# Kernel optimization log

Hardware: AMD Instinct MI355X
Metric: run time of the kernel (lower is better)

## Reference

```python
import jax, jax.numpy as jnp
import numpy as np


def setup_inputs() -> dict:
    key = jax.random.key(0)
    ks = jax.random.split(key, 16)
    N, F_in, C, E = 50000, 128, 64, 800000
    H = 2 * C      # hidden width of first GCN layer = 128
    P = 128        # num_proj_hidden
    K = 3          # cluster_num (hardcoded in GRACE)

    def lin(kw, fan_in, fan_out):
        # torch Linear default init: U(-1/sqrt(fan_in), 1/sqrt(fan_in))
        bound = 1.0 / np.sqrt(fan_in)
        return jax.random.uniform(kw, (fan_in, fan_out), jnp.float32, -bound, bound)

    inp = {
        "x1": jax.random.normal(ks[0], (N, F_in), jnp.float32),
        "edge_index1": jax.random.randint(ks[1], (2, E), 0, N, jnp.int64 if jax.config.jax_enable_x64 else jnp.int32),
        "x2": jax.random.normal(ks[2], (N, F_in), jnp.float32),
        "edge_index2": jax.random.randint(ks[3], (2, E), 0, N, jnp.int64 if jax.config.jax_enable_x64 else jnp.int32),
        # encoder GCN layers
        "W1": lin(ks[4], F_in, H), "b1": jnp.zeros((H,), jnp.float32),
        "W2": lin(ks[5], H, C),    "b2": jnp.zeros((C,), jnp.float32),
        # instance projector: Linear(C,C) -> ReLU -> Linear(C,P)
        "Wp1": lin(ks[6], C, C), "bp1": jnp.zeros((C,), jnp.float32),
        "Wp2": lin(ks[7], C, P), "bp2": jnp.zeros((P,), jnp.float32),
        # cluster projector: Linear(C,C) -> ReLU -> Linear(C,K) -> Softmax
        "Wc1": lin(ks[8], C, C), "bc1": jnp.zeros((C,), jnp.float32),
        "Wc2": lin(ks[9], C, K), "bc2": jnp.zeros((K,), jnp.float32),
    }
    return inp


def _gcn_encoder(x, edge_index, W1, b1, W2, b2):
    N = x.shape[0]
    loop = jnp.arange(N, dtype=edge_index.dtype)
    row = jnp.concatenate([edge_index[0], loop])  # message sources (x_j)
    col = jnp.concatenate([edge_index[1], loop])  # aggregation targets
    deg = jax.ops.segment_sum(jnp.ones_like(col, jnp.float32), col, num_segments=N)
    dinv = jax.lax.rsqrt(deg)  # deg >= 1 due to self loops
    norm = dinv[row] * dinv[col]  # [E+N]

    def layer(h, W, b):
        h = h @ W  # transform first (PyG GCNConv), [N, F_out]
        msg = h[row] * norm[:, None]  # gather + scale, [E+N, F_out]
        return jax.ops.segment_sum(msg, col, num_segments=N) + b

    h = jax.nn.relu(layer(x, W1, b1))
    h = jax.nn.relu(layer(h, W2, b2))
    return h


def _l2norm(z, eps=1e-12):
    # matches F.normalize(z, dim=1): x / max(||x||, eps)
    n = jnp.sqrt(jnp.sum(z * z, axis=1, keepdims=True))
    return z / jnp.maximum(n, eps)


def reference(x1, edge_index1, x2, edge_index2,
              W1, b1, W2, b2, Wp1, bp1, Wp2, bp2, Wc1, bc1, Wc2, bc2):
    z1 = _gcn_encoder(x1, edge_index1, W1, b1, W2, b2)
    z2 = _gcn_encoder(x2, edge_index2, W1, b1, W2, b2)

    inst = lambda z: _l2norm(jax.nn.relu(z @ Wp1 + bp1) @ Wp2 + bp2)
    clus = lambda z: jax.nn.softmax(jax.nn.relu(z @ Wc1 + bc1) @ Wc2 + bc2, axis=1)

    z_i = inst(z1)
    z_j = inst(z2)
    c_i = clus(z1)
    c_j = clus(z2)
    return (z_i, z_j, c_i, c_j)
```

## Files before the change

### kernel.cpp

```cpp
#include <hip/hip_runtime.h>
#include <cstdint>
#include <cstddef>

using u16 = unsigned short;
using u32 = unsigned int;

typedef __bf16 bf16x8 __attribute__((ext_vector_type(8)));
typedef float  f32x4  __attribute__((ext_vector_type(4)));

__device__ __forceinline__ float bf2f(u16 b) { union { u32 i; float f; } v; v.i = ((u32)b) << 16; return v.f; }
__device__ __forceinline__ u16 f2bf(float f) { __bf16 b = (__bf16)f; return __builtin_bit_cast(u16, b); }
__device__ __forceinline__ float bflo(u32 u) { union { u32 i; float f; } v; v.i = u << 16; return v.f; }
__device__ __forceinline__ float bfhi(u32 u) { union { u32 i; float f; } v; v.i = u & 0xffff0000u; return v.f; }
__device__ __forceinline__ u32 pack2(float a, float b) { return (u32)f2bf(a) | ((u32)f2bf(b) << 16); }

__device__ __forceinline__ float loadx(const void* p, size_t i, int flag_bf16) {
    return flag_bf16 ? bf2f(((const u16*)p)[i]) : ((const float*)p)[i];
}
__device__ __forceinline__ void storex(void* p, size_t i, float v, int flag_bf16) {
    if (flag_bf16) ((u16*)p)[i] = f2bf(v);
    else           ((float*)p)[i] = v;
}

__device__ __forceinline__ bf16x8 load_afrag_ext(const void* A, size_t off, int flag) {
    if (flag) return *reinterpret_cast<const bf16x8*>((const u16*)A + off);
    const float* f = (const float*)A + off;
    float4 a = *reinterpret_cast<const float4*>(f);
    float4 b = *reinterpret_cast<const float4*>(f + 4);
    bf16x8 r;
    r[0] = (__bf16)a.x; r[1] = (__bf16)a.y; r[2] = (__bf16)a.z; r[3] = (__bf16)a.w;
    r[4] = (__bf16)b.x; r[5] = (__bf16)b.y; r[6] = (__bf16)b.z; r[7] = (__bf16)b.w;
    return r;
}

__global__ void k_detect(const u32* __restrict__ x, int* __restrict__ flag) {
    int lane = threadIdx.x;
    u32 u = x[lane];
    int e = (u >> 7) & 0xFF;
    int hit = (e >= 100 && e <= 145) ? 1 : 0;
    unsigned long long b = __ballot(hit);
    if (lane == 0) flag[0] = (__popcll(b) >= 32) ? 1 : 0;
}

struct ConvJob { const void* src; float* dst; int n; };
struct ConvJobs { ConvJob j[12]; };

__global__ void k_wconv(ConvJobs jobs, const int* __restrict__ flagp) {
    const int f = *flagp;
    const int stride = gridDim.x * blockDim.x;
    for (int s = 0; s < 12; ++s) {
        const ConvJob jb = jobs.j[s];
        for (int i = blockIdx.x * blockDim.x + threadIdx.x; i < jb.n; i += stride)
            jb.dst[i] = loadx(jb.src, i, f);
    }
}

struct TJob { const float* W; u16* WT; int K, NC; };
struct TJobs { TJob j[5]; };

__global__ void k_wtrans(TJobs jobs) {
    const int stride = gridDim.x * blockDim.x;
    for (int s = 0; s < 5; ++s) {
        const TJob jb = jobs.j[s];
        const int tot = jb.K * jb.NC;
        for (int i = blockIdx.x * blockDim.x + threadIdx.x; i < tot; i += stride) {
            int k = i / jb.NC, n = i - k * jb.NC;
            jb.WT[n * jb.K + k] = f2bf(jb.W[i]);
        }
    }
}

static const int CAPSH = 12;
static const int OVCAP = 65536;

__global__ __launch_bounds__(256) void k_bin(const int* __restrict__ ei0, const int* __restrict__ ei1,
                                             int* __restrict__ cur, u32* __restrict__ stage,
                                             int2* __restrict__ ov, int* __restrict__ ocnt,
                                             int E, int NB, int nblk) {
    const int g = blockIdx.y;
    const int* ei = g ? ei1 : ei0;
    const int chunk = (E + nblk - 1) / nblk;
    const int e0 = blockIdx.x * chunk;
    const int e1 = (e0 + chunk < E) ? e0 + chunk : E;
    const int tid = threadIdx.x;
    __shared__ int h[512];
    __shared__ int lb[512];
    for (int i = tid; i < NB; i += 256) h[i] = 0;
    __syncthreads();
    for (int e = e0 + tid; e < e1; e += 256) {
        int d = __builtin_nontemporal_load(ei + E + e);
        atomicAdd(&h[d >> 7], 1);
    }
    __syncthreads();
    for (int b = tid; b < NB; b += 256) {
        int c = h[b];
        lb[b] = c ? atomicAdd(&cur[g * NB + b], c) : 0;
    }
    __syncthreads();
    for (int i = tid; i < NB; i += 256) h[i] = 0;
    __syncthreads();
    for (int e = e0 + tid; e < e1; e += 256) {
        int s = __builtin_nontemporal_load(ei + e);
        int d = ei[E + e];
        int b = d >> 7;
        int p = lb[b] + atomicAdd(&h[b], 1);
        if (p < (1 << CAPSH)) {
            stage[((size_t)(g * NB + b) << CAPSH) + p] = (u32)s | ((u32)(d & 127) << 16);
        } else {
            int oi = atomicAdd(ocnt, 1);
            if (oi < OVCAP) ov[oi] = make_int2(s, d | (g << 24));
        }
    }
}

__global__ __launch_bounds__(256) void k_bscan(const int* __restrict__ cur, const int2* __restrict__ ov,
                                               const int* __restrict__ ocnt, int* __restrict__ bbase,
                                               int* __restrict__ rowptr, int N, int E, int NB) {
    __shared__ int tot[2][512];
    const int tid = threadIdx.x;
    for (int g = 0; g < 2; ++g)
        for (int i = tid; i < 512; i += 256) {
            int s = 0;
            if (i < NB) {
                int cv = cur[g * NB + i];
                s = (cv < (1 << CAPSH)) ? cv : (1 << CAPSH);
            }
            tot[g][i] = s;
        }
    __syncthreads();
    int no = *ocnt; if (no > OVCAP) no = OVCAP;
    for (int i = tid; i < no; i += 256) {
        int y = ov[i].y;
        atomicAdd(&tot[y >> 24][(y & 0xFFFFFF) >> 7], 1);
    }
    __syncthreads();
    int o00 = tot[0][tid], o01 = tot[0][tid + 256];
    int o10 = tot[1][tid], o11 = tot[1][tid + 256];
    for (int off = 1; off < 512; off <<= 1) {
        int a0 = tot[0][tid]       + ((tid >= off)       ? tot[0][tid - off]       : 0);
        int a1 = tot[0][tid + 256] + ((tid + 256 >= off) ? tot[0][tid + 256 - off] : 0);
        int b0 = tot[1][tid]       + ((tid >= off)       ? tot[1][tid - off]       : 0);
        int b1 = tot[1][tid + 256] + ((tid + 256 >= off) ? tot[1][tid + 256 - off] : 0);
        __syncthreads();
        tot[0][tid] = a0; tot[0][tid + 256] = a1;
        tot[1][tid] = b0; tot[1][tid + 256] = b1;
        __syncthreads();
    }
    if (tid < NB)       { bbase[tid]            = tot[0][tid] - o00;       bbase[NB + tid]       = tot[1][tid] - o10; }
    if (tid + 256 < NB) { bbase[tid + 256]      = tot[0][tid + 256] - o01; bbase[NB + tid + 256] = tot[1][tid + 256] - o11; }
    if (tid == 0) {
        rowptr[N] = E;
        rowptr[(size_t)(N + 1) + N] = E;
    }
}

__global__ __launch_bounds__(256) void k_scatter(const int* __restrict__ cur, const u32* __restrict__ stage,
                                                 const int2* __restrict__ ov, const int* __restrict__ ocnt,
                                                 const int* __restrict__ bbase, int* __restrict__ rowptr,
                                                 float* __restrict__ dinv, int* __restrict__ csr,
                                                 int N, int E, int NB) {
    const int g = blockIdx.y, b = blockIdx.x, tid = threadIdx.x;
    const int lo = b << 7;
    int R = N - lo; if (R > 128) R = 128;
    __shared__ int hist[128], scn[128], curs[128];
    if (tid < 128) hist[tid] = 0;
    __syncthreads();
    int cv = cur[g * NB + b];
    const int n = (cv < (1 << CAPSH)) ? cv : (1 << CAPSH);
    const u32* sp = stage + ((size_t)(g * NB + b) << CAPSH);
    for (int i = tid; i < n; i += 256) atomicAdd(&hist[sp[i] >> 16], 1);
    int no = *ocnt; if (no > OVCAP) no = OVCAP;
    for (int i = tid; i < no; i += 256) {
        int y = ov[i].y;
        if ((y >> 24) != g) continue;
        int d = y & 0xFFFFFF;
        if (d >= lo && d < lo + 128) atomicAdd(&hist[d - lo], 1);
    }
    __syncthreads();
    int orig = (tid < 128) ? hist[tid] : 0;
    if (tid < 128) scn[tid] = orig;
    __syncthreads();
    for (int off = 1; off < 128; off <<= 1) {
        int v = 0;
        if (tid < 128) v = scn[tid] + ((tid >= off) ? scn[tid - off] : 0);
        __syncthreads();
        if (tid < 128) scn[tid] = v;
        __syncthreads();
    }
    const int base = bbase[g * NB + b];
    if (tid < R) {
        int ex = base + scn[tid] - orig;
        rowptr[(size_t)g * (N + 1) + lo + tid] = ex;
        curs[tid] = ex;
        dinv[(size_t)g * N + lo + tid] = rsqrtf((float)(orig + 1));
    }
    __syncthreads();
    int* out = csr + (size_t)g * E;
    for (int i = tid; i < n; i += 256) {
        u32 v = sp[i];
        int pos = atomicAdd(&curs[v >> 16], 1);
        out[pos] = (int)(v & 0xFFFFu);
    }
    for (int i = tid; i < no; i += 256) {
        int y = ov[i].y;
        if ((y >> 24) != g) continue;
        int d = y & 0xFFFFFF;
        if (d >= lo && d < lo + 128) {
            int pos = atomicAdd(&curs[d - lo], 1);
            out[pos] = ov[i].x;
        }
    }
}

template <int K, int NC, bool AEXT, bool BIAS, bool RELU, bool NORM, bool OEXT>
__global__ __launch_bounds__(256) void k_mgemm(const void* __restrict__ A0, const void* __restrict__ A1,
                                               size_t astride, const u16* __restrict__ WT,
                                               const float* __restrict__ bias, void* __restrict__ outv,
                                               size_t out_off, size_t ostride, int M,
                                               const int* __restrict__ flagp) {
    constexpr int NT = NC / 16;
    constexpr int KI = K / 32;
    const int flag = *flagp;
    const int g = blockIdx.y;
    const void* Av = g ? A1 : A0;
    const int lane = threadIdx.x & 63;
    const int wave = threadIdx.x >> 6;
    const int q = lane >> 4;
    const int c = lane & 15;
    const int m0 = blockIdx.x * 64 + wave * 16;
    int arow = m0 + c;
    if (arow > M - 1) arow = M - 1;
    const size_t abase = (size_t)g * astride + (size_t)arow * K;

    bf16x8 afr[KI];
#pragma unroll
    for (int ki = 0; ki < KI; ++ki) {
        size_t off = abase + (size_t)ki * 32 + q * 8;
        if (AEXT) afr[ki] = load_afrag_ext(Av, off, flag);
        else      afr[ki] = *reinterpret_cast<const bf16x8*>((const u16*)Av + off);
    }

    f32x4 acc[NT];
#pragma unroll
    for (int t = 0; t < NT; ++t) acc[t] = (f32x4){0.f, 0.f, 0.f, 0.f};

#pragma unroll
    for (int ki = 0; ki < KI; ++ki) {
#pragma unroll
        for (int t = 0; t < NT; ++t) {
            const u16* bptr = WT + (size_t)(t * 16 + c) * K + ki * 32 + q * 8;
            bf16x8 bfr = *reinterpret_cast<const bf16x8*>(bptr);
            acc[t] = __builtin_amdgcn_mfma_f32_16x16x32_bf16(afr[ki], bfr, acc[t], 0, 0, 0);
        }
    }

#pragma unroll
    for (int t = 0; t < NT; ++t) {
        float bv = BIAS ? bias[t * 16 + c] : 0.f;
#pragma unroll
        for (int r = 0; r < 4; ++r) {
            float v = acc[t][r] + bv;
            if (RELU) v = fmaxf(v, 0.f);
            acc[t][r] = v;
        }
    }

    if constexpr (NORM) {
        float ss[4] = {0.f, 0.f, 0.f, 0.f};
#pragma unroll
        for (int t = 0; t < NT; ++t)
#pragma unroll
            for (int r = 0; r < 4; ++r) ss[r] += acc[t][r] * acc[t][r];
#pragma unroll
        for (int r = 0; r < 4; ++r) {
#pragma unroll
            for (int m = 1; m < 16; m <<= 1) ss[r] += __shfl_xor(ss[r], m, 64);
            float s = 1.f / fmaxf(sqrtf(ss[r]), 1e-12f);
#pragma unroll
            for (int t = 0; t < NT; ++t) acc[t][r] *= s;
        }
    }

    const size_t obase = out_off + (size_t)g * ostride;
#pragma unroll
    for (int r = 0; r < 4; ++r) {
        const int grow = m0 + q * 4 + r;
        if (grow < M) {
#pragma unroll
            for (int t = 0; t < NT; ++t) {
                size_t oi = obase + (size_t)grow * NC + t * 16 + c;
                if (OEXT) storex(outv, oi, acc[t][r], flag);
                else      ((u16*)outv)[oi] = f2bf(acc[t][r]);
            }
        }
    }
}

__global__ __launch_bounds__(256) void k_agg128(const u32* __restrict__ H, const int* __restrict__ rowptr,
                                                const int* __restrict__ csr, const float* __restrict__ dinv,
                                                const float* __restrict__ bias, u32* __restrict__ out,
                                                int N, int E) {
    const int g = blockIdx.y;
    const int node = blockIdx.x * 4 + (threadIdx.x >> 6);
    if (node >= N) return;
    const int lane = threadIdx.x & 63;
    const u32* h = H + (size_t)g * N * 64;
    const int* rp = rowptr + (size_t)g * (N + 1);
    const int* cs = csr + (size_t)g * E;
    const float* dv = dinv + (size_t)g * N;
    const float dn = dv[node];
    int e = rp[node];
    const int end = rp[node + 1];
    u32 su = h[(size_t)node * 64 + lane];
    float w = dn * dn;
    float a0 = bflo(su) * w, a1 = bfhi(su) * w;
    while (e + 8 <= end) {
        int sx[8];
#pragma unroll
        for (int j = 0; j < 8; ++j) sx[j] = cs[e + j];
        u32 hv[8]; float ws[8];
#pragma unroll
        for (int j = 0; j < 8; ++j) { hv[j] = h[(size_t)sx[j] * 64 + lane]; ws[j] = dv[sx[j]]; }
#pragma unroll
        for (int j = 0; j < 8; ++j) {
            float wj = ws[j] * dn;
            a0 += bflo(hv[j]) * wj;
            a1 += bfhi(hv[j]) * wj;
        }
        e += 8;
    }
    while (e + 2 <= end) {
        int s0 = cs[e], s1 = cs[e + 1];
        u32 h0 = h[(size_t)s0 * 64 + lane];
        u32 h1 = h[(size_t)s1 * 64 + lane];
        float w0 = dv[s0] * dn, w1 = dv[s1] * dn;
        a0 += bflo(h0) * w0; a1 += bfhi(h0) * w0;
        a0 += bflo(h1) * w1; a1 += bfhi(h1) * w1;
        e += 2;
    }
    if (e < end) {
        int s0 = cs[e];
        float w0 = dv[s0] * dn;
        u32 h0 = h[(size_t)s0 * 64 + lane];
        a0 += bflo(h0) * w0; a1 += bfhi(h0) * w0;
    }
    a0 = fmaxf(a0 + bias[2 * lane], 0.f);
    a1 = fmaxf(a1 + bias[2 * lane + 1], 0.f);
    out[((size_t)g * N + node) * 64 + lane] = pack2(a0, a1);
}

__global__ __launch_bounds__(256) void k_agg64(const u16* __restrict__ H, const int* __restrict__ rowptr,
                                               const int* __restrict__ csr, const float* __restrict__ dinv,
                                               const float* __restrict__ bias, u16* __restrict__ out,
                                               int N, int E) {
    const int g = blockIdx.y;
    const int node = blockIdx.x * 4 + (threadIdx.x >> 6);
    if (node >= N) return;
    const int lane = threadIdx.x & 63;
    const u16* h = H + (size_t)g * N * 64;
    const int* rp = rowptr + (size_t)g * (N + 1);
    const int* cs = csr + (size_t)g * E;
    const float* dv = dinv + (size_t)g * N;
    const float dn = dv[node];
    int e = rp[node];
    const int end = rp[node + 1];
    float a0 = bf2f(h[(size_t)node * 64 + lane]) * dn * dn;
    while (e + 8 <= end) {
        int sx[8];
#pragma unroll
        for (int j = 0; j < 8; ++j) sx[j] = cs[e + j];
        u16 hv[8]; float ws[8];
#pragma unroll
        for (int j = 0; j < 8; ++j) { hv[j] = h[(size_t)sx[j] * 64 + lane]; ws[j] = dv[sx[j]]; }
#pragma unroll
        for (int j = 0; j < 8; ++j) a0 += bf2f(hv[j]) * (ws[j] * dn);
        e += 8;
    }
    while (e + 2 <= end) {
        int s0 = cs[e], s1 = cs[e + 1];
        float h0 = bf2f(h[(size_t)s0 * 64 + lane]);
        float h1 = bf2f(h[(size_t)s1 * 64 + lane]);
        a0 += h0 * (dv[s0] * dn) + h1 * (dv[s1] * dn);
        e += 2;
    }
    if (e < end) {
        int s0 = cs[e];
        a0 += bf2f(h[(size_t)s0 * 64 + lane]) * (dv[s0] * dn);
    }
    a0 = fmaxf(a0 + bias[lane], 0.f);
    out[((size_t)g * N + node) * 64 + lane] = f2bf(a0);
}

__global__ __launch_bounds__(256) void k_clus(const u16* __restrict__ v, const float* __restrict__ Wc2,
                                              const float* __restrict__ bc2, void* __restrict__ outv,
                                              size_t out_off, size_t ostride, int N,
                                              const int* __restrict__ flagp) {
    const int g = blockIdx.y;
    const int node = blockIdx.x * 4 + (threadIdx.x >> 6);
    if (node >= N) return;
    const int flag = *flagp;
    const int lane = threadIdx.x & 63;
    float ul = bf2f(v[((size_t)g * N + node) * 64 + lane]);
    float a0 = ul * Wc2[lane * 3 + 0];
    float a1 = ul * Wc2[lane * 3 + 1];
    float a2 = ul * Wc2[lane * 3 + 2];
#pragma unroll
    for (int m = 1; m < 64; m <<= 1) {
        a0 += __shfl_xor(a0, m, 64);
        a1 += __shfl_xor(a1, m, 64);
        a2 += __shfl_xor(a2, m, 64);
    }
    a0 += bc2[0]; a1 += bc2[1]; a2 += bc2[2];
    float mx = fmaxf(a0, fmaxf(a1, a2));
    float e0 = expf(a0 - mx), e1 = expf(a1 - mx), e2 = expf(a2 - mx);
    float inv = 1.f / (e0 + e1 + e2);
    if (lane < 3) {
        float r = (lane == 0) ? e0 : ((lane == 1) ? e1 : e2);
        storex(outv, out_off + (size_t)g * ostride + (size_t)node * 3 + lane, r * inv, flag);
    }
}

extern "C" void kernel_launch(void* const* d_in, const int* in_sizes, int n_in,
                              void* d_out, int out_size, void* d_ws, size_t ws_size,
                              hipStream_t stream) {
    const int N = in_sizes[0] / 128;
    const int E = in_sizes[1] / 2;
    const int* ei0 = (const int*)d_in[1];
    const int* ei1 = (const int*)d_in[3];
    const int NB = (N + 127) >> 7;

    size_t off = 0;
    auto alloc = [&](size_t bytes) -> void* {
        void* p = (char*)d_ws + off;
        off += (bytes + 255) & ~(size_t)255;
        return p;
    };
    int* flag = (int*)alloc(256);
    const int wcnt[12] = {128 * 128, 128, 128 * 64, 64, 64 * 64, 64, 64 * 128, 128, 64 * 64, 64, 64 * 3, 3};
    float* wf[12];
    for (int i = 0; i < 12; ++i) wf[i] = (float*)alloc((size_t)wcnt[i] * 4);
    float* b1f = wf[1]; float* b2f = wf[3]; float* bp1f = wf[5]; float* bp2f = wf[7];
    float* bc1f = wf[9]; float* Wc2f = wf[10]; float* bc2f = wf[11];
    u16* W1T  = (u16*)alloc(128 * 128 * 2);
    u16* W2T  = (u16*)alloc(64 * 128 * 2);
    u16* Wp1T = (u16*)alloc(64 * 64 * 2);
    u16* Wp2T = (u16*)alloc(128 * 64 * 2);
    u16* Wc1T = (u16*)alloc(64 * 64 * 2);

    const int ncell = 2 * NB;
    int* cur    = (int*)alloc((size_t)(ncell + 1) * 4);
    int* ocnt   = cur + ncell;
    int2* ov    = (int2*)alloc((size_t)OVCAP * 8);
    u32* stage  = (u32*)alloc(((size_t)ncell << CAPSH) * 4);
    int* bbase  = (int*)alloc((size_t)2 * NB * 4);
    int* rowptr = (int*)alloc((size_t)2 * (N + 1) * 4);
    float* dinv = (float*)alloc((size_t)2 * N * 4);
    int* csr    = (int*)alloc((size_t)2 * E * 4);
    u16* A1 = (u16*)alloc((size_t)2 * N * 128 * 2);
    u16* H2 = A1;
    u16* Qb = (u16*)alloc((size_t)2 * N * 128 * 2);
    u16* U  = Qb;
    u16* Z  = (u16*)alloc((size_t)2 * N * 64 * 2);
    (void)ws_size; (void)n_in; (void)out_size;

    k_detect<<<1, 64, 0, stream>>>((const u32*)d_in[0], flag);
    ConvJobs jobs;
    for (int i = 0; i < 12; ++i) jobs.j[i] = ConvJob{d_in[4 + i], wf[i], wcnt[i]};
    k_wconv<<<64, 256, 0, stream>>>(jobs, flag);
    TJobs tj;
    tj.j[0] = TJob{wf[0], W1T, 128, 128};
    tj.j[1] = TJob{wf[2], W2T, 128, 64};
    tj.j[2] = TJob{wf[4], Wp1T, 64, 64};
    tj.j[3] = TJob{wf[6], Wp2T, 64, 128};
    tj.j[4] = TJob{wf[8], Wc1T, 64, 64};
    k_wtrans<<<40, 256, 0, stream>>>(tj);

    hipMemsetAsync(cur, 0, (size_t)(ncell + 1) * 4, stream);
    const int NBLK = 128;
    k_bin<<<dim3(NBLK, 2), 256, 0, stream>>>(ei0, ei1, cur, stage, ov, ocnt, E, NB, NBLK);
    k_bscan<<<1, 256, 0, stream>>>(cur, ov, ocnt, bbase, rowptr, N, E, NB);
    k_scatter<<<dim3(NB, 2), 256, 0, stream>>>(cur, stage, ov, ocnt, bbase, rowptr, dinv, csr, N, E, NB);

    const dim3 gM((N + 63) / 64, 2);
    const dim3 gA((N + 3) / 4, 2);

    k_mgemm<128, 128, true, false, false, false, false><<<gM, 256, 0, stream>>>(
        d_in[0], d_in[2], 0, W1T, nullptr, A1, 0, (size_t)N * 128, N, flag);
    k_agg128<<<gA, 256, 0, stream>>>((const u32*)A1, rowptr, csr, dinv, b1f, (u32*)Qb, N, E);
    k_mgemm<128, 64, false, false, false, false, false><<<gM, 256, 0, stream>>>(
        Qb, Qb, (size_t)N * 128, W2T, nullptr, H2, 0, (size_t)N * 64, N, flag);
    k_agg64<<<gA, 256, 0, stream>>>(H2, rowptr, csr, dinv, b2f, Z, N, E);

    k_mgemm<64, 64, false, true, true, false, false><<<gM, 256, 0, stream>>>(
        Z, Z, (size_t)N * 64, Wp1T, bp1f, U, 0, (size_t)N * 64, N, flag);
    k_mgemm<64, 128, false, true, false, true, true><<<gM, 256, 0, stream>>>(
        U, U, (size_t)N * 64, Wp2T, bp2f, d_out, 0, (size_t)N * 128, N, flag);
    k_mgemm<64, 64, false, true, true, false, false><<<gM, 256, 0, stream>>>(
        Z, Z, (size_t)N * 64, Wc1T, bc1f, U, 0, (size_t)N * 64, N, flag);
    k_clus<<<gA, 256, 0, stream>>>(U, Wc2f, bc2f, d_out,
                                   (size_t)2 * N * 128, (size_t)N * 3, N, flag);
}
```

Measured before the change: 428.1 us.

## Prescale GEMM outputs by dinv and cooperatively load CSR indices in aggregation

Folds the source-side normalization dinv[src] into the epilogue of the preceding GEMMs, so the aggregation kernels sum raw neighbor rows and multiply by dinv[dst] once at the end. This removes the per-edge random gather of dinv and the per-edge multiply. The aggregation kernels also load up to 64 neighbor indices with one coalesced wave load and broadcast them by shuffle, instead of each lane re-reading the same indices. The cost is bf16 rounding of prescaled values and a small extra dinv read in the GEMM epilogue.

```diff
diff --git a/kernel.cpp b/kernel.cpp
--- a/kernel.cpp
+++ b/kernel.cpp
@@ -212,12 +212,13 @@
     }
 }
 
-template <int K, int NC, bool AEXT, bool BIAS, bool RELU, bool NORM, bool OEXT>
+template <int K, int NC, bool AEXT, bool BIAS, bool RELU, bool NORM, bool OEXT, bool SCALE>
 __global__ __launch_bounds__(256) void k_mgemm(const void* __restrict__ A0, const void* __restrict__ A1,
                                                size_t astride, const u16* __restrict__ WT,
                                                const float* __restrict__ bias, void* __restrict__ outv,
                                                size_t out_off, size_t ostride, int M,
-                                               const int* __restrict__ flagp) {
+                                               const int* __restrict__ flagp,
+                                               const float* __restrict__ dvp) {
     constexpr int NT = NC / 16;
     constexpr int KI = K / 32;
     const int flag = *flagp;
@@ -286,11 +287,14 @@
     for (int r = 0; r < 4; ++r) {
         const int grow = m0 + q * 4 + r;
         if (grow < M) {
+            float sc = 1.f;
+            if constexpr (SCALE) sc = dvp[(size_t)g * M + grow];
 #pragma unroll
             for (int t = 0; t < NT; ++t) {
+                float v = SCALE ? acc[t][r] * sc : acc[t][r];
                 size_t oi = obase + (size_t)grow * NC + t * 16 + c;
-                if (OEXT) storex(outv, oi, acc[t][r], flag);
-                else      ((u16*)outv)[oi] = f2bf(acc[t][r]);
+                if (OEXT) storex(outv, oi, v, flag);
+                else      ((u16*)outv)[oi] = f2bf(v);
             }
         }
     }
@@ -307,45 +311,34 @@
     const u32* h = H + (size_t)g * N * 64;
     const int* rp = rowptr + (size_t)g * (N + 1);
     const int* cs = csr + (size_t)g * E;
-    const float* dv = dinv + (size_t)g * N;
-    const float dn = dv[node];
+    const float dn = dinv[(size_t)g * N + node];
     int e = rp[node];
     const int end = rp[node + 1];
     u32 su = h[(size_t)node * 64 + lane];
-    float w = dn * dn;
-    float a0 = bflo(su) * w, a1 = bfhi(su) * w;
-    while (e + 8 <= end) {
-        int sx[8];
-#pragma unroll
-        for (int j = 0; j < 8; ++j) sx[j] = cs[e + j];
-        u32 hv[8]; float ws[8];
-#pragma unroll
-        for (int j = 0; j < 8; ++j) { hv[j] = h[(size_t)sx[j] * 64 + lane]; ws[j] = dv[sx[j]]; }
-#pragma unroll
-        for (int j = 0; j < 8; ++j) {
-            float wj = ws[j] * dn;
-            a0 += bflo(hv[j]) * wj;
-            a1 += bfhi(hv[j]) * wj;
-        }
-        e += 8;
-    }
-    while (e + 2 <= end) {
-        int s0 = cs[e], s1 = cs[e + 1];
-        u32 h0 = h[(size_t)s0 * 64 + lane];
-        u32 h1 = h[(size_t)s1 * 64 + lane];
-        float w0 = dv[s0] * dn, w1 = dv[s1] * dn;
-        a0 += bflo(h0) * w0; a1 += bfhi(h0) * w0;
-        a0 += bflo(h1) * w1; a1 += bfhi(h1) * w1;
-        e += 2;
-    }
-    if (e < end) {
-        int s0 = cs[e];
-        float w0 = dv[s0] * dn;
-        u32 h0 = h[(size_t)s0 * 64 + lane];
-        a0 += bflo(h0) * w0; a1 += bfhi(h0) * w0;
-    }
-    a0 = fmaxf(a0 + bias[2 * lane], 0.f);
-    a1 = fmaxf(a1 + bias[2 * lane + 1], 0.f);
+    float a0 = bflo(su), a1 = bfhi(su);
+    while (e < end) {
+        int cnt = end - e; if (cnt > 64) cnt = 64;
+        int my = (lane < cnt) ? cs[e + lane] : 0;
+        int j = 0;
+        for (; j + 8 <= cnt; j += 8) {
+            int sx[8];
+#pragma unroll
+            for (int k = 0; k < 8; ++k) sx[k] = __shfl(my, j + k, 64);
+            u32 hv[8];
+#pragma unroll
+            for (int k = 0; k < 8; ++k) hv[k] = h[(size_t)sx[k] * 64 + lane];
+#pragma unroll
+            for (int k = 0; k < 8; ++k) { a0 += bflo(hv[k]); a1 += bfhi(hv[k]); }
+        }
+        for (; j < cnt; ++j) {
+            int s = __shfl(my, j, 64);
+            u32 hv = h[(size_t)s * 64 + lane];
+            a0 += bflo(hv); a1 += bfhi(hv);
+        }
+        e += cnt;
+    }
+    a0 = fmaxf(a0 * dn + bias[2 * lane], 0.f);
+    a1 = fmaxf(a1 * dn + bias[2 * lane + 1], 0.f);
     out[((size_t)g * N + node) * 64 + lane] = pack2(a0, a1);
 }
 
@@ -360,34 +353,31 @@
     const u16* h = H + (size_t)g * N * 64;
     const int* rp = rowptr + (size_t)g * (N + 1);
     const int* cs = csr + (size_t)g * E;
-    const float* dv = dinv + (size_t)g * N;
-    const float dn = dv[node];
+    const float dn = dinv[(size_t)g * N + node];
     int e = rp[node];
     const int end = rp[node + 1];
-    float a0 = bf2f(h[(size_t)node * 64 + lane]) * dn * dn;
-    while (e + 8 <= end) {
-        int sx[8];
-#pragma unroll
-        for (int j = 0; j < 8; ++j) sx[j] = cs[e + j];
-        u16 hv[8]; float ws[8];
-#pragma unroll
-        for (int j = 0; j < 8; ++j) { hv[j] = h[(size_t)sx[j] * 64 + lane]; ws[j] = dv[sx[j]]; }
-#pragma unroll
-        for (int j = 0; j < 8; ++j) a0 += bf2f(hv[j]) * (ws[j] * dn);
-        e += 8;
-    }
-    while (e + 2 <= end) {
-        int s0 = cs[e], s1 = cs[e + 1];
-        float h0 = bf2f(h[(size_t)s0 * 64 + lane]);
-        float h1 = bf2f(h[(size_t)s1 * 64 + lane]);
-        a0 += h0 * (dv[s0] * dn) + h1 * (dv[s1] * dn);
-        e += 2;
-    }
-    if (e < end) {
-        int s0 = cs[e];
-        a0 += bf2f(h[(size_t)s0 * 64 + lane]) * (dv[s0] * dn);
-    }
-    a0 = fmaxf(a0 + bias[lane], 0.f);
+    float a0 = bf2f(h[(size_t)node * 64 + lane]);
+    while (e < end) {
+        int cnt = end - e; if (cnt > 64) cnt = 64;
+        int my = (lane < cnt) ? cs[e + lane] : 0;
+        int j = 0;
+        for (; j + 8 <= cnt; j += 8) {
+            int sx[8];
+#pragma unroll
+            for (int k = 0; k < 8; ++k) sx[k] = __shfl(my, j + k, 64);
+            u16 hv[8];
+#pragma unroll
+            for (int k = 0; k < 8; ++k) hv[k] = h[(size_t)sx[k] * 64 + lane];
+#pragma unroll
+            for (int k = 0; k < 8; ++k) a0 += bf2f(hv[k]);
+        }
+        for (; j < cnt; ++j) {
+            int s = __shfl(my, j, 64);
+            a0 += bf2f(h[(size_t)s * 64 + lane]);
+        }
+        e += cnt;
+    }
+    a0 = fmaxf(a0 * dn + bias[lane], 0.f);
     out[((size_t)g * N + node) * 64 + lane] = f2bf(a0);
 }
 
@@ -484,19 +474,19 @@
     const dim3 gM((N + 63) / 64, 2);
     const dim3 gA((N + 3) / 4, 2);
 
-    k_mgemm<128, 128, true, false, false, false, false><<<gM, 256, 0, stream>>>(
-        d_in[0], d_in[2], 0, W1T, nullptr, A1, 0, (size_t)N * 128, N, flag);
+    k_mgemm<128, 128, true, false, false, false, false, true><<<gM, 256, 0, stream>>>(
+        d_in[0], d_in[2], 0, W1T, nullptr, A1, 0, (size_t)N * 128, N, flag, dinv);
     k_agg128<<<gA, 256, 0, stream>>>((const u32*)A1, rowptr, csr, dinv, b1f, (u32*)Qb, N, E);
-    k_mgemm<128, 64, false, false, false, false, false><<<gM, 256, 0, stream>>>(
-        Qb, Qb, (size_t)N * 128, W2T, nullptr, H2, 0, (size_t)N * 64, N, flag);
+    k_mgemm<128, 64, false, false, false, false, false, true><<<gM, 256, 0, stream>>>(
+        Qb, Qb, (size_t)N * 128, W2T, nullptr, H2, 0, (size_t)N * 64, N, flag, dinv);
     k_agg64<<<gA, 256, 0, stream>>>(H2, rowptr, csr, dinv, b2f, Z, N, E);
 
-    k_mgemm<64, 64, false, true, true, false, false><<<gM, 256, 0, stream>>>(
-        Z, Z, (size_t)N * 64, Wp1T, bp1f, U, 0, (size_t)N * 64, N, flag);
-    k_mgemm<64, 128, false, true, false, true, true><<<gM, 256, 0, stream>>>(
-        U, U, (size_t)N * 64, Wp2T, bp2f, d_out, 0, (size_t)N * 128, N, flag);
-    k_mgemm<64, 64, false, true, true, false, false><<<gM, 256, 0, stream>>>(
-        Z, Z, (size_t)N * 64, Wc1T, bc1f, U, 0, (size_t)N * 64, N, flag);
+    k_mgemm<64, 64, false, true, true, false, false, false><<<gM, 256, 0, stream>>>(
+        Z, Z, (size_t)N * 64, Wp1T, bp1f, U, 0, (size_t)N * 64, N, flag, nullptr);
+    k_mgemm<64, 128, false, true, false, true, true, false><<<gM, 256, 0, stream>>>(
+        U, U, (size_t)N * 64, Wp2T, bp2f, d_out, 0, (size_t)N * 128, N, flag, nullptr);
+    k_mgemm<64, 64, false, true, true, false, false, false><<<gM, 256, 0, stream>>>(
+        Z, Z, (size_t)N * 64, Wc1T, bc1f, U, 0, (size_t)N * 64, N, flag, nullptr);
     k_clus<<<gA, 256, 0, stream>>>(U, Wc2f, bc2f, d_out,
                                    (size_t)2 * N * 128, (size_t)N * 3, N, flag);
 }
```

New measurement: 423.8 us. Within noise of the previous version (-1.0%).
